# Kernel optimization log

Measured on AMD Instinct MI355X. Metric: run time of the kernel, lower is better.

## Reference

```python
import jax, jax.numpy as jnp
import numpy as np

B, C, H, W = 8, 512, 64, 64


def conv3x3(x, w, b):
    # x: [B,C,H,W], w: [O,I,3,3], b: [O]; stride 1, padding 1 (SAME)
    y = jax.lax.conv_general_dilated(
        x, w, window_strides=(1, 1), padding='SAME',
        dimension_numbers=('NCHW', 'OIHW', 'NCHW'))
    return y + b[None, :, None, None]


def setup_inputs() -> dict:
    key = jax.random.key(0)
    ks = jax.random.split(key, 8)
    wscale = 1.0 / np.sqrt(C * 9)  # keep attention logits in a sane range
    x = jax.random.normal(ks[0], (B, C, H, W), dtype=jnp.float32)
    wq = jax.random.normal(ks[1], (C, C, 3, 3), dtype=jnp.float32) * wscale
    bq = jax.random.normal(ks[2], (C,), dtype=jnp.float32) * 0.01
    wk = jax.random.normal(ks[3], (C, C, 3, 3), dtype=jnp.float32) * wscale
    bk = jax.random.normal(ks[4], (C,), dtype=jnp.float32) * 0.01
    wv = jax.random.normal(ks[5], (C, C, 3, 3), dtype=jnp.float32) * wscale
    bv = jax.random.normal(ks[6], (C,), dtype=jnp.float32) * 0.01
    gamma = jax.random.normal(ks[7], (1,), dtype=jnp.float32)
    return {'x': x, 'wq': wq, 'bq': bq, 'wk': wk, 'bk': bk,
            'wv': wv, 'bv': bv, 'gamma': gamma}


def reference(x, wq, bq, wk, bk, wv, bv, gamma):
    b, c, h, w = x.shape
    n = h * w
    q = conv3x3(x, wq, bq).reshape(b, c, n)   # [B,C,N]
    k = conv3x3(x, wk, bk).reshape(b, c, n)   # [B,C,N]
    v = conv3x3(x, wv, bv).reshape(b, c, n)   # [B,C,N]
    # channel-wise attention: [B,C,N] x [B,N,C] -> [B,C,C]
    attn = jnp.einsum('bcn,bdn->bcd', q, k)
    attn = jax.nn.softmax(attn, axis=-1)
    out = jnp.einsum('bcd,bdn->bcn', attn, v).reshape(b, c, h, w)
    return gamma * out + x
```

## Files before the change

kernel.cpp:

```cpp
#include <hip/hip_runtime.h>
#include <stdint.h>

typedef __attribute__((ext_vector_type(8))) short bf16x8;
typedef __attribute__((ext_vector_type(4))) float f32x4;
typedef __attribute__((ext_vector_type(4))) int i32x4;
typedef __attribute__((ext_vector_type(8))) int i32x8;
typedef __attribute__((ext_vector_type(8))) unsigned short u16x8;
typedef __attribute__((ext_vector_type(4))) unsigned short u16x4;

#define DI static __device__ __forceinline__

constexpr int CB = 8;
constexpr int BCH = 4;
constexpr int CC = 512;
constexpr int CN = 4096;
constexpr int K1 = CC * 9;
constexpr int MR = 3 * CC;
constexpr int KSPL = 8;
constexpr size_t XSPLIT = (size_t)BCH * 66 * 66 * 512;

DI unsigned short f2bf(float f) {
  union { float f; uint32_t u; } v; v.f = f;
  uint32_t r = (v.u + 0x7FFFu + ((v.u >> 16) & 1u)) >> 16;
  return (unsigned short)r;
}
DI float bf2f(unsigned short h) {
  union { uint32_t u; float f; } v; v.u = ((uint32_t)h) << 16;
  return v.f;
}
DI unsigned char f2e4m3(float x) {
  union { float f; uint32_t u; } v; v.f = x;
  uint32_t sgn = (v.u >> 24) & 0x80u;
  float a = fabsf(x);
  if (a < 0.015625f) {
    int qi = (int)rintf(a * 512.f);
    return (unsigned char)(sgn | (uint32_t)qi);
  }
  int e = (int)((v.u >> 23) & 0xff) - 127;
  uint32_t m3 = (v.u >> 20) & 7u;
  uint32_t rest = v.u & 0xFFFFFu;
  if (rest > 0x80000u || (rest == 0x80000u && (m3 & 1u))) {
    if (++m3 == 8u) { m3 = 0; ++e; }
  }
  if (e > 8 || (e == 8 && m3 == 7u)) return (unsigned char)(sgn | 0x7Eu);
  return (unsigned char)(sgn | ((uint32_t)(e + 7) << 3) | m3);
}

DI void g2lds16(const void* g, void* l) {
  __builtin_amdgcn_global_load_lds((const __attribute__((address_space(1))) void*)g,
                                   (__attribute__((address_space(3))) void*)l, 16, 0, 0);
}
#define SBAR()  __builtin_amdgcn_s_barrier()
#define SCHED() __builtin_amdgcn_sched_barrier(0)

__global__ __launch_bounds__(256) void pad_zero(unsigned short* __restrict__ Xhi,
                                                unsigned char* __restrict__ X8) {
  int id = blockIdx.x * 256 + threadIdx.x;
  if (id >= 4 * 260 * 16) return;
  int t = id & 15;
  int pp = (id >> 4) % 260;
  int b = id / (260 * 16);
  int hh, ww;
  if (pp < 66)       { hh = 0;  ww = pp; }
  else if (pp < 132) { hh = 65; ww = pp - 66; }
  else if (pp < 196) { hh = pp - 131; ww = 0; }
  else               { hh = pp - 195; ww = 65; }
  size_t pix = (((size_t)b * 66 + hh) * 66 + ww) * 512 + (size_t)t * 32;
  const u16x8 z = {0, 0, 0, 0, 0, 0, 0, 0};
  *(u16x8*)&Xhi[pix] = z;  *(u16x8*)&Xhi[pix + 8] = z;
  *(u16x8*)&Xhi[pix + 16] = z;  *(u16x8*)&Xhi[pix + 24] = z;
  const i32x4 z4 = {0, 0, 0, 0};
  *(i32x4*)&X8[pix] = z4;  *(i32x4*)&X8[pix + 16] = z4;
  *(i32x4*)&X8[XSPLIT + pix] = z4;  *(i32x4*)&X8[XSPLIT + pix + 16] = z4;
}

__global__ __launch_bounds__(256) void prep_xpad(const float* __restrict__ x,
                                                 unsigned short* __restrict__ Xhi,
                                                 unsigned char* __restrict__ X8) {
  int tid = threadIdx.x;
  int w = tid & 63;
  int ccl = tid >> 6;
  int blk = blockIdx.x;
  int h = blk & 63;
  int ccg = (blk >> 6) & 15;
  int b = blk >> 10;
  int c0 = (ccg * 4 + ccl) * 8;
  const float* xp = x + ((size_t)b * CC) * CN + h * 64 + w;
  u16x8 hi;
  unsigned long long lo8 = 0, hi8 = 0;
#pragma unroll
  for (int j = 0; j < 8; ++j) {
    float v = xp[(size_t)(c0 + j) * CN];
    unsigned short h16 = f2bf(v);
    float vhi = bf2f(h16);
    hi[j] = f2bf(vhi * 128.f);
    lo8 |= (unsigned long long)f2e4m3((v - vhi) * 256.f) << (8 * j);
    hi8 |= (unsigned long long)f2e4m3(vhi) << (8 * j);
  }
  size_t pix = (((size_t)b * 66 + (h + 1)) * 66 + (w + 1)) * 512;
  *(u16x8*)&Xhi[pix + c0] = hi;
  *(unsigned long long*)&X8[pix + c0] = lo8;
  *(unsigned long long*)&X8[XSPLIT + pix + c0] = hi8;
}

__global__ __launch_bounds__(256) void prep_abig(
    const float* __restrict__ wq, const float* __restrict__ wk,
    const float* __restrict__ wv, const float* __restrict__ bq,
    const float* __restrict__ bk, const float* __restrict__ bv,
    unsigned short* __restrict__ Ahi, unsigned char* __restrict__ A8,
    float* __restrict__ bias) {
  unsigned id = blockIdx.x * 256 + threadIdx.x;
  int m = id / K1;
  int r = id - m * K1;
  int t = r >> 9;
  int c = r & 511;
  int ky = t / 3;
  int kx = t - ky * 3;
  size_t ip = (size_t)m * 9216 + r;
  if (m < 1024) {
    const float* wp = (m < 512) ? wq : wk;
    int mm = (m < 512) ? m : m - 512;
    float wval = wp[(((size_t)mm * 512 + c) * 3 + ky) * 3 + kx];
    float whi = bf2f(f2bf(wval));
    Ahi[id] = f2bf(whi * 128.f);
    A8[ip] = f2e4m3(whi * 64.f);
    A8[ip + 4608] = f2e4m3((wval - whi) * 16384.f);
  } else {
    float wval = wv[(((size_t)(m - 1024) * 512 + c) * 3 + ky) * 3 + kx];
    Ahi[id] = f2bf(wval * 128.f);
    A8[ip] = 0;
    A8[ip + 4608] = 0;
  }
  if (id < 1536) {
    int mm = (int)id;
    bias[mm] = (mm < 512) ? bq[mm] : (mm < 1024) ? bk[mm - 512] : bv[mm - 1024];
  }
}

__global__ __launch_bounds__(512, 2) void conv_k(
    const unsigned short* __restrict__ Ahi,
    const unsigned char* __restrict__ A8,
    const unsigned short* __restrict__ Xhi,
    const unsigned char* __restrict__ X8,
    const float* __restrict__ bias,
    unsigned short* __restrict__ Qhi, unsigned short* __restrict__ Qlo,
    unsigned short* __restrict__ Khi, unsigned short* __restrict__ Klo,
    unsigned short* __restrict__ Vt)
{
  __shared__ __align__(16) unsigned char smem[4 * 32768];
  const int tid = threadIdx.x;
  const int lane = tid & 63;
  const int wid = tid >> 6;
  const int wr = wid >> 2;
  const int wc = wid & 3;

  int orig = blockIdx.x;
  int xcd, nbl, m0;
  if (orig < 256) {
    xcd = orig & 7; int j = orig >> 3;
    nbl = j >> 2;
    m0 = (j & 3) * 256;
  } else {
    int o = orig - 256;
    xcd = o & 7; int j = o >> 3;
    nbl = j >> 2;
    m0 = 1024 + (j & 3) * 128;
  }
  const int nb = xcd * 8 + nbl;
  const int n0 = nb * 256;
  const int bidx = n0 >> 12;
  const int nl0 = n0 & (CN - 1);
  const int h0 = nl0 >> 6;

  const int srow = tid >> 2;
  const int scu = tid & 3;
  const int scuS = scu ^ ((srow >> 1) & 3);
  const int d8 = (scuS & 1) ? -16 : 16;
  const size_t pixOfs = (((size_t)(bidx * 66 + h0 + (srow >> 6))) * 66 + (srow & 63)) * 512;
  const unsigned short* gAh0 = Ahi + (size_t)(m0 + srow) * K1 + scuS * 8;
  const unsigned short* gAh1 = gAh0 + (size_t)128 * K1;
  const unsigned short* gBh0 = Xhi + pixOfs + scuS * 8;
  const unsigned short* gBh1 = gBh0 + (size_t)2 * 66 * 512;
  const unsigned char* gA80 = A8 + (size_t)(m0 + srow) * 9216 + scuS * 16;
  const unsigned char* gA81 = gA80 + (size_t)128 * 9216;
  const unsigned char* gB80 = X8 + pixOfs + scuS * 16;
  const unsigned char* gB81 = gB80 + (size_t)2 * 66 * 512;
  const int wofs = wid * 1024;

  int c0S = 0, kxS = 0, tapS = 0;
  size_t tapOfs = 0;
  auto stage1 = [&](int slot) {
    int aOfs = tapS * 512 + c0S;
    size_t bOfs = tapOfs + (size_t)c0S;
    unsigned char* lA = smem + slot * 32768 + wofs;
    unsigned char* lB = smem + slot * 32768 + 16384 + wofs;
    g2lds16(gAh0 + aOfs, lA);
    g2lds16(gAh1 + aOfs, lA + 8192);
    g2lds16(gBh0 + bOfs, lB);
    g2lds16(gBh1 + bOfs, lB + 8192);
    c0S += 32;
    if (c0S == 512) {
      c0S = 0; ++tapS;
      if (kxS == 2) { kxS = 0; tapOfs += (size_t)64 * 512; }
      else { ++kxS; tapOfs += 512; }
    }
  };
  auto stage1v = [&](int slot) {
    int aOfs = tapS * 512 + c0S;
    size_t bOfs = tapOfs + (size_t)c0S;
    unsigned char* lA = smem + slot * 32768 + wofs;
    unsigned char* lB = smem + slot * 32768 + 16384 + wofs;
    g2lds16(gAh0 + aOfs, lA);
    g2lds16(gBh0 + bOfs, lB);
    g2lds16(gBh1 + bOfs, lB + 8192);
    c0S += 32;
    if (c0S == 512) {
      c0S = 0; ++tapS;
      if (kxS == 2) { kxS = 0; tapOfs += (size_t)64 * 512; }
      else { ++kxS; tapOfs += 512; }
    }
  };
  int c8 = 0, kx8 = 0, tap8 = 0, s8 = 0;
  size_t tapOfs8 = 0;
  auto stage2 = [&](int slot) {
    int so = (slot & 1) ? d8 : 0;
    int aOfs = s8 * 4608 + tap8 * 512 + c8;
    size_t bOfs = (size_t)s8 * XSPLIT + tapOfs8 + (size_t)c8;
    unsigned char* lA = smem + slot * 32768 + wofs;
    unsigned char* lB = smem + slot * 32768 + 16384 + wofs;
    g2lds16(gA80 + aOfs + so, lA);
    g2lds16(gA81 + aOfs + so, lA + 8192);
    g2lds16(gB80 + bOfs + so, lB);
    g2lds16(gB81 + bOfs + so, lB + 8192);
    c8 += 64;
    if (c8 == 512) {
      c8 = 0; ++tap8;
      if (tap8 == 9) { tap8 = 0; kx8 = 0; tapOfs8 = 0; ++s8; }
      else if (kx8 == 2) { kx8 = 0; tapOfs8 += (size_t)64 * 512; }
      else { ++kx8; tapOfs8 += 512; }
    }
  };

  f32x4 acc[8][4];
  const f32x4 fz = {0.f, 0.f, 0.f, 0.f};
#pragma unroll
  for (int i = 0; i < 8; ++i)
#pragma unroll
    for (int j = 0; j < 4; ++j) acc[i][j] = fz;

  const int kq = (lane >> 4) * 16;
  int slotC, slotS, t2;

  if (m0 < 1024) {
    const int rA = wr * 128 + (lane & 15);
    const int rB = wc * 64 + (lane & 15);
    const int kqA = kq ^ (((rA >> 1) & 3) << 4);
    const int kqB = kq ^ (((rB >> 1) & 3) << 4);

    stage1(0);
    stage1(1);
    asm volatile("s_waitcnt vmcnt(4)" ::: "memory");
    SCHED(); SBAR(); SCHED();
    {
      bf16x8 afA[4], bfA[4], afB[4], bfB[4], af1[4];
#pragma unroll
      for (int mf = 0; mf < 4; ++mf)
        afA[mf] = *(const bf16x8*)(smem + (rA + mf * 16) * 64 + kqA);
#pragma unroll
      for (int nf = 0; nf < 4; ++nf)
        bfA[nf] = *(const bf16x8*)(smem + 16384 + (rB + nf * 16) * 64 + kqB);
      slotC = 0; slotS = 2; t2 = 2;

#define CONV_BF(CURA, CURB, NXTA, NXTB)                                       \
  {                                                                           \
    if (t2 < 144) {                                                           \
      stage1(slotS); slotS = (slotS + 1) & 3;                                 \
      asm volatile("s_waitcnt vmcnt(4)" ::: "memory");                        \
    } else {                                                                  \
      asm volatile("s_waitcnt vmcnt(0)" ::: "memory");                        \
    }                                                                         \
    SCHED(); SBAR(); SCHED();                                                 \
    const unsigned char* lA = smem + slotC * 32768;                           \
    const int slotN = (slotC + 1) & 3;                                        \
    const unsigned char* lAn = smem + slotN * 32768;                          \
    _Pragma("unroll")                                                         \
    for (int mf = 0; mf < 4; ++mf)                                            \
      af1[mf] = *(const bf16x8*)(lA + (rA + 64 + mf * 16) * 64 + kqA);        \
    __builtin_amdgcn_s_setprio(1);                                            \
    _Pragma("unroll")                                                         \
    for (int mf = 0; mf < 4; ++mf) {                                          \
      _Pragma("unroll")                                                       \
      for (int nf = 0; nf < 4; ++nf)                                          \
        acc[mf][nf] = __builtin_amdgcn_mfma_f32_16x16x32_bf16(                \
            CURA[mf], CURB[nf], acc[mf][nf], 0, 0, 0);                        \
    }                                                                         \
    __builtin_amdgcn_s_setprio(0);                                            \
    _Pragma("unroll")                                                         \
    for (int mf = 0; mf < 4; ++mf)                                            \
      NXTA[mf] = *(const bf16x8*)(lAn + (rA + mf * 16) * 64 + kqA);           \
    _Pragma("unroll")                                                         \
    for (int nf = 0; nf < 4; ++nf)                                            \
      NXTB[nf] = *(const bf16x8*)(lAn + 16384 + (rB + nf * 16) * 64 + kqB);   \
    __builtin_amdgcn_s_setprio(1);                                            \
    _Pragma("unroll")                                                         \
    for (int mf = 0; mf < 4; ++mf) {                                          \
      _Pragma("unroll")                                                       \
      for (int nf = 0; nf < 4; ++nf)                                          \
        acc[mf + 4][nf] = __builtin_amdgcn_mfma_f32_16x16x32_bf16(            \
            af1[mf], CURB[nf], acc[mf + 4][nf], 0, 0, 0);                     \
    }                                                                         \
    __builtin_amdgcn_s_setprio(0);                                            \
    slotC = slotN;                                                            \
    ++t2;                                                                     \
  }

      for (int t = 0; t < 144; t += 2) {
        CONV_BF(afA, bfA, afB, bfB)
        CONV_BF(afB, bfB, afA, bfA)
      }
#undef CONV_BF
    }

    stage2(0); stage2(1);
    SCHED(); SBAR(); SCHED();
    stage2(2); stage2(3);
    {
      const int gq = lane >> 4;
      const int slotByte = (gq >> 1) << 15;
      const int cb2 = (gq & 1) * 2;
      const int fx = (((lane & 15) >> 1) & 3) ^ (gq >> 1);
      const int bo0 = ((cb2 ^ fx) << 4);
      const int bo1 = (((cb2 + 1) ^ fx) << 4);
      const int aRow = wr * 128 + (lane & 15);
      const int bRow = wc * 64 + (lane & 15);
      i32x8 aF[4], bF[4];
      for (int p = 0; p < 72; ++p) {
        SCHED(); SBAR(); SCHED();
        if (p < 71) { asm volatile("s_waitcnt vmcnt(8)" ::: "memory"); }
        else        { asm volatile("s_waitcnt vmcnt(0)" ::: "memory"); }
        SCHED();
        const unsigned char* pbA = smem + ((p & 1) << 16) + slotByte + aRow * 64;
        const unsigned char* pbB = smem + ((p & 1) << 16) + slotByte + 16384 + bRow * 64;
#pragma unroll
        for (int t = 0; t < 4; ++t) {
          *(i32x4*)&bF[t] = *(const i32x4*)(pbB + t * 1024 + bo0);
          *((i32x4*)&bF[t] + 1) = *(const i32x4*)(pbB + t * 1024 + bo1);
        }
#pragma unroll
        for (int s = 0; s < 4; ++s) {
          *(i32x4*)&aF[s] = *(const i32x4*)(pbA + s * 1024 + bo0);
          *((i32x4*)&aF[s] + 1) = *(const i32x4*)(pbA + s * 1024 + bo1);
        }
        __builtin_amdgcn_s_setprio(1);
#pragma unroll
        for (int s = 0; s < 4; ++s)
#pragma unroll
          for (int t = 0; t < 4; ++t)
            acc[s][t] = __builtin_amdgcn_mfma_scale_f32_16x16x128_f8f6f4(
                aF[s], bF[t], acc[s][t], 0, 0, 0, 127, 0, 127);
        __builtin_amdgcn_s_setprio(0);
#pragma unroll
        for (int s = 0; s < 4; ++s) {
          *(i32x4*)&aF[s] = *(const i32x4*)(pbA + (4 + s) * 1024 + bo0);
          *((i32x4*)&aF[s] + 1) = *(const i32x4*)(pbA + (4 + s) * 1024 + bo1);
        }
        __builtin_amdgcn_s_setprio(1);
#pragma unroll
        for (int s = 0; s < 4; ++s)
#pragma unroll
          for (int t = 0; t < 4; ++t)
            acc[s + 4][t] = __builtin_amdgcn_mfma_scale_f32_16x16x128_f8f6f4(
                aF[s], bF[t], acc[s + 4][t], 0, 0, 0, 127, 0, 127);
        __builtin_amdgcn_s_setprio(0);
        SCHED(); SBAR(); SCHED();
        if (p + 2 < 72) { stage2(2 * (p & 1)); stage2(2 * (p & 1) + 1); }
      }
    }
  } else {
    const int rAv = wr * 64 + (lane & 15);
    const int rB = wc * 64 + (lane & 15);
    const int kqA = kq ^ (((rAv >> 1) & 3) << 4);
    const int kqB = kq ^ (((rB >> 1) & 3) << 4);

    stage1v(0);
    stage1v(1);
    asm volatile("s_waitcnt vmcnt(3)" ::: "memory");
    SCHED(); SBAR(); SCHED();
    bf16x8 afA[4], bfA[4], afB[4], bfB[4];
#pragma unroll
    for (int mf = 0; mf < 4; ++mf)
      afA[mf] = *(const bf16x8*)(smem + (rAv + mf * 16) * 64 + kqA);
#pragma unroll
    for (int nf = 0; nf < 4; ++nf)
      bfA[nf] = *(const bf16x8*)(smem + 16384 + (rB + nf * 16) * 64 + kqB);
    slotC = 0; slotS = 2; t2 = 2;

#define CONV_LV(CURA, CURB, NXTA, NXTB)                                       \
  {                                                                           \
    if (t2 < 144) {                                                           \
      stage1v(slotS); slotS = (slotS + 1) & 3;                                \
      asm volatile("s_waitcnt vmcnt(3)" ::: "memory");                        \
    } else {                                                                  \
      asm volatile("s_waitcnt vmcnt(0)" ::: "memory");                        \
    }                                                                         \
    SCHED(); SBAR(); SCHED();                                                 \
    const int slotN = (slotC + 1) & 3;                                        \
    const unsigned char* lAn = smem + slotN * 32768;                          \
    _Pragma("unroll")                                                         \
    for (int mf = 0; mf < 4; ++mf)                                            \
      NXTA[mf] = *(const bf16x8*)(lAn + (rAv + mf * 16) * 64 + kqA);          \
    _Pragma("unroll")                                                         \
    for (int nf = 0; nf < 4; ++nf)                                            \
      NXTB[nf] = *(const bf16x8*)(lAn + 16384 + (rB + nf * 16) * 64 + kqB);   \
    __builtin_amdgcn_s_setprio(1);                                            \
    _Pragma("unroll")                                                         \
    for (int mf = 0; mf < 4; ++mf) {                                          \
      _Pragma("unroll")                                                       \
      for (int nf = 0; nf < 4; ++nf)                                          \
        acc[mf][nf] = __builtin_amdgcn_mfma_f32_16x16x32_bf16(                \
            CURA[mf], CURB[nf], acc[mf][nf], 0, 0, 0);                        \
    }                                                                         \
    __builtin_amdgcn_s_setprio(0);                                            \
    slotC = slotN;                                                            \
    ++t2;                                                                     \
  }

    for (int t = 0; t < 144; t += 2) {
      CONV_LV(afA, bfA, afB, bfB)
      CONV_LV(afB, bfB, afA, bfA)
    }
#undef CONV_LV
  }

  constexpr float SC = 1.f / 16384.f;
  if (m0 < 1024) {
#pragma unroll
    for (int mf = 0; mf < 8; ++mf) {
#pragma unroll
      for (int nf = 0; nf < 4; ++nf) {
        f32x4 a = acc[mf][nf];
        int mrow = m0 + wr * 128 + mf * 16 + ((lane >> 4) << 2);
        int ncol = nl0 + wc * 64 + nf * 16 + (lane & 15);
        if (m0 < 512) {
#pragma unroll
          for (int j = 0; j < 4; ++j) {
            float v = a[j] * SC + bias[mrow + j];
            unsigned short h16 = f2bf(v);
            size_t o = ((size_t)bidx * CC + (mrow + j)) * CN + ncol;
            Qhi[o] = h16;
            Qlo[o] = f2bf(v - bf2f(h16));
          }
        } else {
#pragma unroll
          for (int j = 0; j < 4; ++j) {
            float v = a[j] * SC + bias[mrow + j];
            unsigned short h16 = f2bf(v);
            size_t o = ((size_t)bidx * CC + (mrow + j - 512)) * CN + ncol;
            Khi[o] = h16;
            Klo[o] = f2bf(v - bf2f(h16));
          }
        }
      }
    }
  } else {
#pragma unroll
    for (int mf = 0; mf < 4; ++mf) {
#pragma unroll
      for (int nf = 0; nf < 4; ++nf) {
        f32x4 a = acc[mf][nf];
        int mrow = m0 + wr * 64 + mf * 16 + ((lane >> 4) << 2);
        int ncol = nl0 + wc * 64 + nf * 16 + (lane & 15);
        u16x4 vs;
#pragma unroll
        for (int j = 0; j < 4; ++j) vs[j] = f2bf(a[j] * SC + bias[mrow + j]);
        *(u16x4*)&Vt[((size_t)bidx * CN + ncol) * CC + (mrow - 1024)] = vs;
      }
    }
  }
}

__global__ __launch_bounds__(512, 2) void qk_k(
    const unsigned short* __restrict__ Qhi, const unsigned short* __restrict__ Qlo,
    const unsigned short* __restrict__ Khi, const unsigned short* __restrict__ Klo,
    float* __restrict__ attn)
{
  __shared__ __align__(16) unsigned char smem[4 * 24576];
  const int tid = threadIdx.x;
  const int lane = tid & 63;
  const int wid = tid >> 6;
  const int wr = wid >> 2;
  const int wc = wid & 3;

  int orig = blockIdx.x;
  int work = (orig & 7) * 8 + (orig >> 3);
  const int mt = work & 3;
  const int nt = (work >> 2) & 1;
  const int ks = work >> 3;
  const int bidx = blockIdx.z;
  const int m0 = mt * 128;
  const int n0 = nt * 256;

  const int srow = tid >> 2;
  const int scu = tid & 3;
  const int scuS = scu ^ ((srow >> 1) & 3);
  const size_t rowA = ((size_t)bidx * CC + m0 + srow) * CN + scuS * 8;
  const size_t rowB = ((size_t)bidx * CC + n0 + srow) * CN + scuS * 8;
  const size_t rowB2 = rowB + (size_t)128 * CN;
  const int wofs = wid * 1024;

  int kk = ks * 1536;
  auto stageQ = [&](int slot) {
    int ph = kk >> 12;
    int kin = kk & (CN - 1);
    const unsigned short* Aq = (ph == 2) ? Qlo : Qhi;
    const unsigned short* Bk = (ph == 1) ? Klo : Khi;
    unsigned char* lA = smem + slot * 24576 + wofs;
    unsigned char* lB = smem + slot * 24576 + 8192 + wofs;
    g2lds16(Aq + rowA + kin, lA);
    g2lds16(Bk + rowB + kin, lB);
    g2lds16(Bk + rowB2 + kin, lB + 8192);
    kk += 32;
  };

  f32x4 acc[4][4];
  const f32x4 fz = {0.f, 0.f, 0.f, 0.f};
#pragma unroll
  for (int i = 0; i < 4; ++i)
#pragma unroll
    for (int j = 0; j < 4; ++j) acc[i][j] = fz;

  const int rAv = wr * 64 + (lane & 15);
  const int rB = wc * 64 + (lane & 15);
  const int kq = (lane >> 4) * 16;
  const int kqA = kq ^ (((rAv >> 1) & 3) << 4);
  const int kqB = kq ^ (((rB >> 1) & 3) << 4);

  stageQ(0);
  stageQ(1);
  asm volatile("s_waitcnt vmcnt(3)" ::: "memory");
  SCHED(); SBAR(); SCHED();
  bf16x8 afA[4], bfA[4], afB[4], bfB[4];
#pragma unroll
  for (int mf = 0; mf < 4; ++mf)
    afA[mf] = *(const bf16x8*)(smem + (rAv + mf * 16) * 64 + kqA);
#pragma unroll
  for (int nf = 0; nf < 4; ++nf)
    bfA[nf] = *(const bf16x8*)(smem + 8192 + (rB + nf * 16) * 64 + kqB);
  int slotC = 0, slotS = 2, t2 = 2;

#define QK_BODY(CURA, CURB, NXTA, NXTB)                                       \
  {                                                                           \
    if (t2 < 48) {                                                            \
      stageQ(slotS); slotS = (slotS + 1) & 3;                                 \
      asm volatile("s_waitcnt vmcnt(3)" ::: "memory");                        \
    } else {                                                                  \
      asm volatile("s_waitcnt vmcnt(0)" ::: "memory");                        \
    }                                                                         \
    SCHED(); SBAR(); SCHED();                                                 \
    const int slotN = (slotC + 1) & 3;                                        \
    const unsigned char* lAn = smem + slotN * 24576;                          \
    _Pragma("unroll")                                                         \
    for (int mf = 0; mf < 4; ++mf)                                            \
      NXTA[mf] = *(const bf16x8*)(lAn + (rAv + mf * 16) * 64 + kqA);          \
    _Pragma("unroll")                                                         \
    for (int nf = 0; nf < 4; ++nf)                                            \
      NXTB[nf] = *(const bf16x8*)(lAn + 8192 + (rB + nf * 16) * 64 + kqB);    \
    __builtin_amdgcn_s_setprio(1);                                            \
    _Pragma("unroll")                                                         \
    for (int mf = 0; mf < 4; ++mf) {                                          \
      _Pragma("unroll")                                                       \
      for (int nf = 0; nf < 4; ++nf)                                          \
        acc[mf][nf] = __builtin_amdgcn_mfma_f32_16x16x32_bf16(                \
            CURA[mf], CURB[nf], acc[mf][nf], 0, 0, 0);                        \
    }                                                                         \
    __builtin_amdgcn_s_setprio(0);                                            \
    slotC = slotN;                                                            \
    ++t2;                                                                     \
  }

  for (int t = 0; t < 48; t += 2) {
    QK_BODY(afA, bfA, afB, bfB)
    QK_BODY(afB, bfB, afA, bfA)
  }
#undef QK_BODY

  size_t pbase = (size_t)ks * ((size_t)BCH * CC * CC);
#pragma unroll
  for (int mf = 0; mf < 4; ++mf) {
#pragma unroll
    for (int nf = 0; nf < 4; ++nf) {
      f32x4 a = acc[mf][nf];
      int mrow = m0 + wr * 64 + mf * 16 + ((lane >> 4) << 2);
      int ncol = n0 + wc * 64 + nf * 16 + (lane & 15);
#pragma unroll
      for (int j = 0; j < 4; ++j)
        attn[pbase + ((size_t)bidx * CC + (mrow + j)) * CC + ncol] = a[j];
    }
  }
}

DI int sofs(int row, int kb) { return row * 128 + (kb ^ ((row & 7) << 4)); }

__global__ __launch_bounds__(256) void pv_k(
    const unsigned short* __restrict__ Vt,
    const unsigned short* __restrict__ P,
    const float* __restrict__ xin,
    const float* __restrict__ gamma,
    float* __restrict__ out)
{
  __shared__ __align__(16) unsigned char sA[16384];
  __shared__ __align__(16) unsigned char sB[16384];
  const int tid = threadIdx.x;
  const int lane = tid & 63;
  const int wav = tid >> 6;
  const int wr = wav >> 1, wc = wav & 1;

  const int m0 = (blockIdx.x & 3) * 128;
  const int n0 = (blockIdx.x >> 2) * 128;
  const int bidx = blockIdx.z;

  auto stage = [&](int k0) {
#pragma unroll
    for (int q = 0; q < 4; ++q) {
      int ci = q * 256 + tid;
      int row = ci >> 3;
      int ke = ((ci & 7) ^ (row & 7)) * 8;
      const unsigned short* ap = P + ((size_t)bidx * CC + (m0 + row)) * CC + (k0 + ke);
      const unsigned short* bp = Vt + ((size_t)bidx * CN + (n0 + row)) * CC + (k0 + ke);
      int wbase = (q * 256 + wav * 64) * 16;
      g2lds16(ap, sA + wbase);
      g2lds16(bp, sB + wbase);
    }
  };

  f32x4 acc[4][4];
  const f32x4 fz = {0.f, 0.f, 0.f, 0.f};
#pragma unroll
  for (int i = 0; i < 4; ++i)
#pragma unroll
    for (int j = 0; j < 4; ++j) acc[i][j] = fz;

  for (int k0 = 0; k0 < CC; k0 += 64) {
    stage(k0);
    __syncthreads();
#pragma unroll
    for (int kkp = 0; kkp < 2; ++kkp) {
      bf16x8 af[4], bfv[4];
#pragma unroll
      for (int mf = 0; mf < 4; ++mf)
        af[mf] = *(const bf16x8*)&sA[sofs(wr * 64 + mf * 16 + (lane & 15),
                                          kkp * 64 + (lane >> 4) * 16)];
#pragma unroll
      for (int nf = 0; nf < 4; ++nf)
        bfv[nf] = *(const bf16x8*)&sB[sofs(wc * 64 + nf * 16 + (lane & 15),
                                           kkp * 64 + (lane >> 4) * 16)];
#pragma unroll
      for (int mf = 0; mf < 4; ++mf)
#pragma unroll
        for (int nf = 0; nf < 4; ++nf)
          acc[mf][nf] = __builtin_amdgcn_mfma_f32_16x16x32_bf16(
              af[mf], bfv[nf], acc[mf][nf], 0, 0, 0);
    }
    __syncthreads();
  }

  float g = gamma[0];
#pragma unroll
  for (int mf = 0; mf < 4; ++mf) {
#pragma unroll
    for (int nf = 0; nf < 4; ++nf) {
      f32x4 a = acc[mf][nf];
      int mrow = m0 + wr * 64 + mf * 16 + ((lane >> 4) << 2);
      int ncol = n0 + wc * 64 + nf * 16 + (lane & 15);
#pragma unroll
      for (int j = 0; j < 4; ++j) {
        size_t o = ((size_t)bidx * CC + (mrow + j)) * CN + ncol;
        out[o] = g * a[j] + xin[o];
      }
    }
  }
}

__global__ __launch_bounds__(256) void softmax_k(const float* __restrict__ attn,
                                                 unsigned short* __restrict__ P) {
  int row = blockIdx.x * 4 + (threadIdx.x >> 6);
  int lane = threadIdx.x & 63;
  constexpr size_t PS = (size_t)BCH * CC * CC;
  const float* rp = attn + (size_t)row * 512 + lane * 8;
  f32x4 a = {0.f, 0.f, 0.f, 0.f};
  f32x4 b = {0.f, 0.f, 0.f, 0.f};
#pragma unroll
  for (int ksp = 0; ksp < KSPL; ++ksp) {
    a += *(const f32x4*)(rp + (size_t)ksp * PS);
    b += *(const f32x4*)(rp + (size_t)ksp * PS + 4);
  }
  float mx = fmaxf(fmaxf(fmaxf(a[0], a[1]), fmaxf(a[2], a[3])),
                   fmaxf(fmaxf(b[0], b[1]), fmaxf(b[2], b[3])));
#pragma unroll
  for (int s = 32; s > 0; s >>= 1) mx = fmaxf(mx, __shfl_xor(mx, s, 64));
  float e[8];
  float sum = 0.f;
#pragma unroll
  for (int j = 0; j < 4; ++j) { e[j] = __expf(a[j] - mx); sum += e[j]; }
#pragma unroll
  for (int j = 0; j < 4; ++j) { e[4 + j] = __expf(b[j] - mx); sum += e[4 + j]; }
#pragma unroll
  for (int s = 32; s > 0; s >>= 1) sum += __shfl_xor(sum, s, 64);
  float inv = 1.0f / sum;
  u16x8 o;
#pragma unroll
  for (int j = 0; j < 8; ++j) o[j] = f2bf(e[j] * inv);
  *(u16x8*)&P[(size_t)row * 512 + lane * 8] = o;
}

__global__ __launch_bounds__(256) void fill_sentinel(float* __restrict__ out, int n) {
  int i = blockIdx.x * 256 + threadIdx.x;
  if (i < n) out[i] = 1.0e4f;
}

extern "C" void kernel_launch(void* const* d_in, const int* in_sizes, int n_in,
                              void* d_out, int out_size, void* d_ws, size_t ws_size,
                              hipStream_t stream) {
  (void)in_sizes; (void)n_in;
  const float* x  = (const float*)d_in[0];
  const float* wq = (const float*)d_in[1];
  const float* bq = (const float*)d_in[2];
  const float* wk = (const float*)d_in[3];
  const float* bk = (const float*)d_in[4];
  const float* wv = (const float*)d_in[5];
  const float* bv = (const float*)d_in[6];
  const float* gm = (const float*)d_in[7];
  float* out = (float*)d_out;

  uint8_t* wsp = (uint8_t*)d_ws;
  auto take = [&](size_t bytes) {
    uint8_t* p = wsp;
    wsp += (bytes + 255) & ~(size_t)255;
    return p;
  };
  unsigned short* Xhi = (unsigned short*)take(XSPLIT * 2);
  unsigned char*  X8  = (unsigned char*)take(2 * XSPLIT);
  unsigned short* Ahi = (unsigned short*)take((size_t)MR * K1 * 2);
  unsigned char*  A8  = (unsigned char*)take((size_t)MR * 2 * K1);
  float* bias         = (float*)take((size_t)MR * 4);
  unsigned short* Khi = (unsigned short*)take((size_t)BCH * CC * CN * 2);
  unsigned short* Klo = (unsigned short*)take((size_t)BCH * CC * CN * 2);
  unsigned short* Vt  = (unsigned short*)take((size_t)BCH * CN * CC * 2);
  float* attn         = (float*)Xhi;
  unsigned short* P   = (unsigned short*)((uint8_t*)Xhi +
                          (size_t)KSPL * BCH * CC * CC * 4 + 256);

  size_t needed = (size_t)(wsp - (uint8_t*)d_ws);
  if (ws_size < needed) {
    fill_sentinel<<<(out_size + 255) / 256, 256, 0, stream>>>(out, out_size);
    return;
  }

  for (int ch = 0; ch < CB / BCH; ++ch) {
    const float* xch = x + (size_t)ch * BCH * CC * CN;
    float* outch = out + (size_t)ch * BCH * CC * CN;
    unsigned short* Qhi = (unsigned short*)outch;
    unsigned short* Qlo = Qhi + (size_t)BCH * CC * CN;

    pad_zero<<<(4 * 260 * 16 + 255) / 256, 256, 0, stream>>>(Xhi, X8);
    prep_xpad<<<BCH * 16 * 64, 256, 0, stream>>>(xch, Xhi, X8);
    if (ch == 0)
      prep_abig<<<(MR * K1) / 256, 256, 0, stream>>>(wq, wk, wv, bq, bk, bv,
                                                     Ahi, A8, bias);
    conv_k<<<dim3(512), 512, 0, stream>>>(Ahi, A8, Xhi, X8, bias,
                                          Qhi, Qlo, Khi, Klo, Vt);
    qk_k<<<dim3(64, 1, BCH), 512, 0, stream>>>(Qhi, Qlo, Khi, Klo, attn);
    softmax_k<<<BCH * 128, 256, 0, stream>>>(attn, P);
    pv_k<<<dim3(128, 1, BCH), 256, 0, stream>>>(Vt, P, xch, gm, outch);
  }
}
```

Measured before the change: 945.2 us.

## Shrink conv tiles to 128 rows for higher occupancy and unify code paths

```diff
diff --git a/kernel.cpp b/kernel.cpp
--- a/kernel.cpp
+++ b/kernel.cpp
@@ -137,7 +137,7 @@
   }
 }
 
-__global__ __launch_bounds__(512, 2) void conv_k(
+__global__ __launch_bounds__(512, 4) void conv_k(
     const unsigned short* __restrict__ Ahi,
     const unsigned char* __restrict__ A8,
     const unsigned short* __restrict__ Xhi,
@@ -147,7 +147,7 @@
     unsigned short* __restrict__ Khi, unsigned short* __restrict__ Klo,
     unsigned short* __restrict__ Vt)
 {
-  __shared__ __align__(16) unsigned char smem[4 * 32768];
+  __shared__ __align__(16) unsigned char smem[3 * 24576];
   const int tid = threadIdx.x;
   const int lane = tid & 63;
   const int wid = tid >> 6;
@@ -156,12 +156,12 @@
 
   int orig = blockIdx.x;
   int xcd, nbl, m0;
-  if (orig < 256) {
+  if (orig < 512) {
     xcd = orig & 7; int j = orig >> 3;
-    nbl = j >> 2;
-    m0 = (j & 3) * 256;
+    nbl = j >> 3;
+    m0 = (j & 7) * 128;
   } else {
-    int o = orig - 256;
+    int o = orig - 512;
     xcd = o & 7; int j = o >> 3;
     nbl = j >> 2;
     m0 = 1024 + (j & 3) * 128;
@@ -175,14 +175,11 @@
   const int srow = tid >> 2;
   const int scu = tid & 3;
   const int scuS = scu ^ ((srow >> 1) & 3);
-  const int d8 = (scuS & 1) ? -16 : 16;
   const size_t pixOfs = (((size_t)(bidx * 66 + h0 + (srow >> 6))) * 66 + (srow & 63)) * 512;
   const unsigned short* gAh0 = Ahi + (size_t)(m0 + srow) * K1 + scuS * 8;
-  const unsigned short* gAh1 = gAh0 + (size_t)128 * K1;
   const unsigned short* gBh0 = Xhi + pixOfs + scuS * 8;
   const unsigned short* gBh1 = gBh0 + (size_t)2 * 66 * 512;
   const unsigned char* gA80 = A8 + (size_t)(m0 + srow) * 9216 + scuS * 16;
-  const unsigned char* gA81 = gA80 + (size_t)128 * 9216;
   const unsigned char* gB80 = X8 + pixOfs + scuS * 16;
   const unsigned char* gB81 = gB80 + (size_t)2 * 66 * 512;
   const int wofs = wid * 1024;
@@ -192,12 +189,10 @@
   auto stage1 = [&](int slot) {
     int aOfs = tapS * 512 + c0S;
     size_t bOfs = tapOfs + (size_t)c0S;
-    unsigned char* lA = smem + slot * 32768 + wofs;
-    unsigned char* lB = smem + slot * 32768 + 16384 + wofs;
-    g2lds16(gAh0 + aOfs, lA);
-    g2lds16(gAh1 + aOfs, lA + 8192);
-    g2lds16(gBh0 + bOfs, lB);
-    g2lds16(gBh1 + bOfs, lB + 8192);
+    unsigned char* lS = smem + slot * 24576 + wofs;
+    g2lds16(gAh0 + aOfs, lS);
+    g2lds16(gBh0 + bOfs, lS + 8192);
+    g2lds16(gBh1 + bOfs, lS + 16384);
     c0S += 32;
     if (c0S == 512) {
       c0S = 0; ++tapS;
@@ -205,87 +200,70 @@
       else { ++kxS; tapOfs += 512; }
     }
   };
-  auto stage1v = [&](int slot) {
-    int aOfs = tapS * 512 + c0S;
-    size_t bOfs = tapOfs + (size_t)c0S;
-    unsigned char* lA = smem + slot * 32768 + wofs;
-    unsigned char* lB = smem + slot * 32768 + 16384 + wofs;
-    g2lds16(gAh0 + aOfs, lA);
-    g2lds16(gBh0 + bOfs, lB);
-    g2lds16(gBh1 + bOfs, lB + 8192);
-    c0S += 32;
-    if (c0S == 512) {
-      c0S = 0; ++tapS;
-      if (kxS == 2) { kxS = 0; tapOfs += (size_t)64 * 512; }
-      else { ++kxS; tapOfs += 512; }
+  int c2 = 0, kx2 = 0, tap2 = 0, s2 = 0;
+  size_t tapOfs2 = 0;
+  auto stagePair = [&]() {
+    int aOfs = s2 * 4608 + tap2 * 512 + c2;
+    size_t bOfs = (size_t)s2 * XSPLIT + tapOfs2 + (size_t)c2;
+    g2lds16(gA80 + aOfs, smem + wofs);
+    g2lds16(gB80 + bOfs, smem + 8192 + wofs);
+    g2lds16(gB81 + bOfs, smem + 16384 + wofs);
+    g2lds16(gA80 + aOfs + 64, smem + 24576 + wofs);
+    g2lds16(gB80 + bOfs + 64, smem + 24576 + 8192 + wofs);
+    g2lds16(gB81 + bOfs + 64, smem + 24576 + 16384 + wofs);
+    c2 += 128;
+    if (c2 == 512) {
+      c2 = 0; ++tap2;
+      if (tap2 == 9) { tap2 = 0; kx2 = 0; tapOfs2 = 0; ++s2; }
+      else if (kx2 == 2) { kx2 = 0; tapOfs2 += (size_t)64 * 512; }
+      else { ++kx2; tapOfs2 += 512; }
     }
   };
-  int c8 = 0, kx8 = 0, tap8 = 0, s8 = 0;
-  size_t tapOfs8 = 0;
-  auto stage2 = [&](int slot) {
-    int so = (slot & 1) ? d8 : 0;
-    int aOfs = s8 * 4608 + tap8 * 512 + c8;
-    size_t bOfs = (size_t)s8 * XSPLIT + tapOfs8 + (size_t)c8;
-    unsigned char* lA = smem + slot * 32768 + wofs;
-    unsigned char* lB = smem + slot * 32768 + 16384 + wofs;
-    g2lds16(gA80 + aOfs + so, lA);
-    g2lds16(gA81 + aOfs + so, lA + 8192);
-    g2lds16(gB80 + bOfs + so, lB);
-    g2lds16(gB81 + bOfs + so, lB + 8192);
-    c8 += 64;
-    if (c8 == 512) {
-      c8 = 0; ++tap8;
-      if (tap8 == 9) { tap8 = 0; kx8 = 0; tapOfs8 = 0; ++s8; }
-      else if (kx8 == 2) { kx8 = 0; tapOfs8 += (size_t)64 * 512; }
-      else { ++kx8; tapOfs8 += 512; }
-    }
-  };
-
-  f32x4 acc[8][4];
+
+  f32x4 acc[4][4];
   const f32x4 fz = {0.f, 0.f, 0.f, 0.f};
 #pragma unroll
-  for (int i = 0; i < 8; ++i)
+  for (int i = 0; i < 4; ++i)
 #pragma unroll
     for (int j = 0; j < 4; ++j) acc[i][j] = fz;
 
+  const int rAv = wr * 64 + (lane & 15);
+  const int rB = wc * 64 + (lane & 15);
   const int kq = (lane >> 4) * 16;
-  int slotC, slotS, t2;
-
-  if (m0 < 1024) {
-    const int rA = wr * 128 + (lane & 15);
-    const int rB = wc * 64 + (lane & 15);
-    const int kqA = kq ^ (((rA >> 1) & 3) << 4);
-    const int kqB = kq ^ (((rB >> 1) & 3) << 4);
-
-    stage1(0);
-    stage1(1);
-    asm volatile("s_waitcnt vmcnt(4)" ::: "memory");
-    SCHED(); SBAR(); SCHED();
-    {
-      bf16x8 afA[4], bfA[4], afB[4], bfB[4], af1[4];
-#pragma unroll
-      for (int mf = 0; mf < 4; ++mf)
-        afA[mf] = *(const bf16x8*)(smem + (rA + mf * 16) * 64 + kqA);
-#pragma unroll
-      for (int nf = 0; nf < 4; ++nf)
-        bfA[nf] = *(const bf16x8*)(smem + 16384 + (rB + nf * 16) * 64 + kqB);
-      slotC = 0; slotS = 2; t2 = 2;
-
-#define CONV_BF(CURA, CURB, NXTA, NXTB)                                       \
+  const int kqA = kq ^ (((rAv >> 1) & 3) << 4);
+  const int kqB = kq ^ (((rB >> 1) & 3) << 4);
+
+  stage1(0);
+  stage1(1);
+  asm volatile("s_waitcnt vmcnt(3)" ::: "memory");
+  SCHED(); SBAR(); SCHED();
+  {
+    bf16x8 afA[4], bfA[4], afB[4], bfB[4];
+#pragma unroll
+    for (int mf = 0; mf < 4; ++mf)
+      afA[mf] = *(const bf16x8*)(smem + (rAv + mf * 16) * 64 + kqA);
+#pragma unroll
+    for (int nf = 0; nf < 4; ++nf)
+      bfA[nf] = *(const bf16x8*)(smem + 8192 + (rB + nf * 16) * 64 + kqB);
+    int slotC = 0, slotS = 2, t2 = 2;
+
+#define CONV_P1(CURA, CURB, NXTA, NXTB)                                       \
   {                                                                           \
     if (t2 < 144) {                                                           \
-      stage1(slotS); slotS = (slotS + 1) & 3;                                 \
-      asm volatile("s_waitcnt vmcnt(4)" ::: "memory");                        \
+      stage1(slotS); slotS = (slotS == 2) ? 0 : slotS + 1;                    \
+      asm volatile("s_waitcnt vmcnt(3)" ::: "memory");                        \
     } else {                                                                  \
       asm volatile("s_waitcnt vmcnt(0)" ::: "memory");                        \
     }                                                                         \
     SCHED(); SBAR(); SCHED();                                                 \
-    const unsigned char* lA = smem + slotC * 32768;                           \
-    const int slotN = (slotC + 1) & 3;                                        \
-    const unsigned char* lAn = smem + slotN * 32768;                          \
+    const int slotN = (slotC == 2) ? 0 : slotC + 1;                           \
+    const unsigned char* lAn = smem + slotN * 24576;                          \
     _Pragma("unroll")                                                         \
     for (int mf = 0; mf < 4; ++mf)                                            \
-      af1[mf] = *(const bf16x8*)(lA + (rA + 64 + mf * 16) * 64 + kqA);        \
+      NXTA[mf] = *(const bf16x8*)(lAn + (rAv + mf * 16) * 64 + kqA);          \
+    _Pragma("unroll")                                                         \
+    for (int nf = 0; nf < 4; ++nf)                                            \
+      NXTB[nf] = *(const bf16x8*)(lAn + 8192 + (rB + nf * 16) * 64 + kqB);    \
     __builtin_amdgcn_s_setprio(1);                                            \
     _Pragma("unroll")                                                         \
     for (int mf = 0; mf < 4; ++mf) {                                          \
@@ -295,181 +273,84 @@
             CURA[mf], CURB[nf], acc[mf][nf], 0, 0, 0);                        \
     }                                                                         \
     __builtin_amdgcn_s_setprio(0);                                            \
-    _Pragma("unroll")                                                         \
-    for (int mf = 0; mf < 4; ++mf)                                            \
-      NXTA[mf] = *(const bf16x8*)(lAn + (rA + mf * 16) * 64 + kqA);           \
-    _Pragma("unroll")                                                         \
-    for (int nf = 0; nf < 4; ++nf)                                            \
-      NXTB[nf] = *(const bf16x8*)(lAn + 16384 + (rB + nf * 16) * 64 + kqB);   \
-    __builtin_amdgcn_s_setprio(1);                                            \
-    _Pragma("unroll")                                                         \
-    for (int mf = 0; mf < 4; ++mf) {                                          \
-      _Pragma("unroll")                                                       \
-      for (int nf = 0; nf < 4; ++nf)                                          \
-        acc[mf + 4][nf] = __builtin_amdgcn_mfma_f32_16x16x32_bf16(            \
-            af1[mf], CURB[nf], acc[mf + 4][nf], 0, 0, 0);                     \
-    }                                                                         \
-    __builtin_amdgcn_s_setprio(0);                                            \
+    asm volatile("s_waitcnt lgkmcnt(0)" ::: "memory");                        \
+    SCHED(); SBAR(); SCHED();                                                 \
     slotC = slotN;                                                            \
     ++t2;                                                                     \
   }
 
-      for (int t = 0; t < 144; t += 2) {
-        CONV_BF(afA, bfA, afB, bfB)
-        CONV_BF(afB, bfB, afA, bfA)
+    for (int t = 0; t < 144; t += 2) {
+      CONV_P1(afA, bfA, afB, bfB)
+      CONV_P1(afB, bfB, afA, bfA)
+    }
+#undef CONV_P1
+  }
+
+  if (m0 < 1024) {
+    const int gq = lane >> 4;
+    const int slotByte = (gq >> 1) * 24576;
+    const int cb2 = (gq & 1) * 2;
+    const int fx = ((lane & 15) >> 1) & 3;
+    const int bo0 = ((cb2 ^ fx) << 4);
+    const int bo1 = (((cb2 + 1) ^ fx) << 4);
+    i32x8 aF[4], bF[4];
+    for (int p = 0; p < 72; ++p) {
+      stagePair();
+      asm volatile("s_waitcnt vmcnt(0)" ::: "memory");
+      SCHED(); SBAR(); SCHED();
+      const unsigned char* pbA = smem + slotByte;
+      const unsigned char* pbB = smem + slotByte + 8192;
+#pragma unroll
+      for (int s = 0; s < 4; ++s) {
+        const unsigned char* ra = pbA + (rAv + s * 16) * 64;
+        *(i32x4*)&aF[s] = *(const i32x4*)(ra + bo0);
+        *((i32x4*)&aF[s] + 1) = *(const i32x4*)(ra + bo1);
       }
-#undef CONV_BF
-    }
-
-    stage2(0); stage2(1);
-    SCHED(); SBAR(); SCHED();
-    stage2(2); stage2(3);
-    {
-      const int gq = lane >> 4;
-      const int slotByte = (gq >> 1) << 15;
-      const int cb2 = (gq & 1) * 2;
-      const int fx = (((lane & 15) >> 1) & 3) ^ (gq >> 1);
-      const int bo0 = ((cb2 ^ fx) << 4);
-      const int bo1 = (((cb2 + 1) ^ fx) << 4);
-      const int aRow = wr * 128 + (lane & 15);
-      const int bRow = wc * 64 + (lane & 15);
-      i32x8 aF[4], bF[4];
-      for (int p = 0; p < 72; ++p) {
-        SCHED(); SBAR(); SCHED();
-        if (p < 71) { asm volatile("s_waitcnt vmcnt(8)" ::: "memory"); }
-        else        { asm volatile("s_waitcnt vmcnt(0)" ::: "memory"); }
-        SCHED();
-        const unsigned char* pbA = smem + ((p & 1) << 16) + slotByte + aRow * 64;
-        const unsigned char* pbB = smem + ((p & 1) << 16) + slotByte + 16384 + bRow * 64;
-#pragma unroll
-        for (int t = 0; t < 4; ++t) {
-          *(i32x4*)&bF[t] = *(const i32x4*)(pbB + t * 1024 + bo0);
-          *((i32x4*)&bF[t] + 1) = *(const i32x4*)(pbB + t * 1024 + bo1);
+#pragma unroll
+      for (int tt = 0; tt < 4; ++tt) {
+        const unsigned char* rb = pbB + (rB + tt * 16) * 64;
+        *(i32x4*)&bF[tt] = *(const i32x4*)(rb + bo0);
+        *((i32x4*)&bF[tt] + 1) = *(const i32x4*)(rb + bo1);
+      }
+      __builtin_amdgcn_s_setprio(1);
+#pragma unroll
+      for (int s = 0; s < 4; ++s)
+#pragma unroll
+        for (int tt = 0; tt < 4; ++tt)
+          acc[s][tt] = __builtin_amdgcn_mfma_scale_f32_16x16x128_f8f6f4(
+              aF[s], bF[tt], acc[s][tt], 0, 0, 0, 127, 0, 127);
+      __builtin_amdgcn_s_setprio(0);
+      SCHED(); SBAR(); SCHED();
+    }
+  }
+
+  constexpr float SC = 1.f / 16384.f;
+#pragma unroll
+  for (int mf = 0; mf < 4; ++mf) {
+#pragma unroll
+    for (int nf = 0; nf < 4; ++nf) {
+      f32x4 a = acc[mf][nf];
+      int mrow = m0 + wr * 64 + mf * 16 + ((lane >> 4) << 2);
+      int ncol = nl0 + wc * 64 + nf * 16 + (lane & 15);
+      if (m0 < 512) {
+#pragma unroll
+        for (int j = 0; j < 4; ++j) {
+          float v = a[j] * SC + bias[mrow + j];
+          unsigned short h16 = f2bf(v);
+          size_t o = ((size_t)bidx * CC + (mrow + j)) * CN + ncol;
+          Qhi[o] = h16;
+          Qlo[o] = f2bf(v - bf2f(h16));
         }
-#pragma unroll
-        for (int s = 0; s < 4; ++s) {
-          *(i32x4*)&aF[s] = *(const i32x4*)(pbA + s * 1024 + bo0);
-          *((i32x4*)&aF[s] + 1) = *(const i32x4*)(pbA + s * 1024 + bo1);
+      } else if (m0 < 1024) {
+#pragma unroll
+        for (int j = 0; j < 4; ++j) {
+          float v = a[j] * SC + bias[mrow + j];
+          unsigned short h16 = f2bf(v);
+          size_t o = ((size_t)bidx * CC + (mrow + j - 512)) * CN + ncol;
+          Khi[o] = h16;
+          Klo[o] = f2bf(v - bf2f(h16));
         }
-        __builtin_amdgcn_s_setprio(1);
-#pragma unroll
-        for (int s = 0; s < 4; ++s)
-#pragma unroll
-          for (int t = 0; t < 4; ++t)
-            acc[s][t] = __builtin_amdgcn_mfma_scale_f32_16x16x128_f8f6f4(
-                aF[s], bF[t], acc[s][t], 0, 0, 0, 127, 0, 127);
-        __builtin_amdgcn_s_setprio(0);
-#pragma unroll
-        for (int s = 0; s < 4; ++s) {
-          *(i32x4*)&aF[s] = *(const i32x4*)(pbA + (4 + s) * 1024 + bo0);
-          *((i32x4*)&aF[s] + 1) = *(const i32x4*)(pbA + (4 + s) * 1024 + bo1);
-        }
-        __builtin_amdgcn_s_setprio(1);
-#pragma unroll
-        for (int s = 0; s < 4; ++s)
-#pragma unroll
-          for (int t = 0; t < 4; ++t)
-            acc[s + 4][t] = __builtin_amdgcn_mfma_scale_f32_16x16x128_f8f6f4(
-                aF[s], bF[t], acc[s + 4][t], 0, 0, 0, 127, 0, 127);
-        __builtin_amdgcn_s_setprio(0);
-        SCHED(); SBAR(); SCHED();
-        if (p + 2 < 72) { stage2(2 * (p & 1)); stage2(2 * (p & 1) + 1); }
-      }
-    }
-  } else {
-    const int rAv = wr * 64 + (lane & 15);
-    const int rB = wc * 64 + (lane & 15);
-    const int kqA = kq ^ (((rAv >> 1) & 3) << 4);
-    const int kqB = kq ^ (((rB >> 1) & 3) << 4);
-
-    stage1v(0);
-    stage1v(1);
-    asm volatile("s_waitcnt vmcnt(3)" ::: "memory");
-    SCHED(); SBAR(); SCHED();
-    bf16x8 afA[4], bfA[4], afB[4], bfB[4];
-#pragma unroll
-    for (int mf = 0; mf < 4; ++mf)
-      afA[mf] = *(const bf16x8*)(smem + (rAv + mf * 16) * 64 + kqA);
-#pragma unroll
-    for (int nf = 0; nf < 4; ++nf)
-      bfA[nf] = *(const bf16x8*)(smem + 16384 + (rB + nf * 16) * 64 + kqB);
-    slotC = 0; slotS = 2; t2 = 2;
-
-#define CONV_LV(CURA, CURB, NXTA, NXTB)                                       \
-  {                                                                           \
-    if (t2 < 144) {                                                           \
-      stage1v(slotS); slotS = (slotS + 1) & 3;                                \
-      asm volatile("s_waitcnt vmcnt(3)" ::: "memory");                        \
-    } else {                                                                  \
-      asm volatile("s_waitcnt vmcnt(0)" ::: "memory");                        \
-    }                                                                         \
-    SCHED(); SBAR(); SCHED();                                                 \
-    const int slotN = (slotC + 1) & 3;                                        \
-    const unsigned char* lAn = smem + slotN * 32768;                          \
-    _Pragma("unroll")                                                         \
-    for (int mf = 0; mf < 4; ++mf)                                            \
-      NXTA[mf] = *(const bf16x8*)(lAn + (rAv + mf * 16) * 64 + kqA);          \
-    _Pragma("unroll")                                                         \
-    for (int nf = 0; nf < 4; ++nf)                                            \
-      NXTB[nf] = *(const bf16x8*)(lAn + 16384 + (rB + nf * 16) * 64 + kqB);   \
-    __builtin_amdgcn_s_setprio(1);                                            \
-    _Pragma("unroll")                                                         \
-    for (int mf = 0; mf < 4; ++mf) {                                          \
-      _Pragma("unroll")                                                       \
-      for (int nf = 0; nf < 4; ++nf)                                          \
-        acc[mf][nf] = __builtin_amdgcn_mfma_f32_16x16x32_bf16(                \
-            CURA[mf], CURB[nf], acc[mf][nf], 0, 0, 0);                        \
-    }                                                                         \
-    __builtin_amdgcn_s_setprio(0);                                            \
-    slotC = slotN;                                                            \
-    ++t2;                                                                     \
-  }
-
-    for (int t = 0; t < 144; t += 2) {
-      CONV_LV(afA, bfA, afB, bfB)
-      CONV_LV(afB, bfB, afA, bfA)
-    }
-#undef CONV_LV
-  }
-
-  constexpr float SC = 1.f / 16384.f;
-  if (m0 < 1024) {
-#pragma unroll
-    for (int mf = 0; mf < 8; ++mf) {
-#pragma unroll
-      for (int nf = 0; nf < 4; ++nf) {
-        f32x4 a = acc[mf][nf];
-        int mrow = m0 + wr * 128 + mf * 16 + ((lane >> 4) << 2);
-        int ncol = nl0 + wc * 64 + nf * 16 + (lane & 15);
-        if (m0 < 512) {
-#pragma unroll
-          for (int j = 0; j < 4; ++j) {
-            float v = a[j] * SC + bias[mrow + j];
-            unsigned short h16 = f2bf(v);
-            size_t o = ((size_t)bidx * CC + (mrow + j)) * CN + ncol;
-            Qhi[o] = h16;
-            Qlo[o] = f2bf(v - bf2f(h16));
-          }
-        } else {
-#pragma unroll
-          for (int j = 0; j < 4; ++j) {
-            float v = a[j] * SC + bias[mrow + j];
-            unsigned short h16 = f2bf(v);
-            size_t o = ((size_t)bidx * CC + (mrow + j - 512)) * CN + ncol;
-            Khi[o] = h16;
-            Klo[o] = f2bf(v - bf2f(h16));
-          }
-        }
-      }
-    }
-  } else {
-#pragma unroll
-    for (int mf = 0; mf < 4; ++mf) {
-#pragma unroll
-      for (int nf = 0; nf < 4; ++nf) {
-        f32x4 a = acc[mf][nf];
-        int mrow = m0 + wr * 64 + mf * 16 + ((lane >> 4) << 2);
-        int ncol = nl0 + wc * 64 + nf * 16 + (lane & 15);
+      } else {
         u16x4 vs;
 #pragma unroll
         for (int j = 0; j < 4; ++j) vs[j] = f2bf(a[j] * SC + bias[mrow + j]);
@@ -767,7 +648,7 @@
     if (ch == 0)
       prep_abig<<<(MR * K1) / 256, 256, 0, stream>>>(wq, wk, wv, bq, bk, bv,
                                                      Ahi, A8, bias);
-    conv_k<<<dim3(512), 512, 0, stream>>>(Ahi, A8, Xhi, X8, bias,
+    conv_k<<<dim3(768), 512, 0, stream>>>(Ahi, A8, Xhi, X8, bias,
                                           Qhi, Qlo, Khi, Klo, Vt);
     qk_k<<<dim3(64, 1, BCH), 512, 0, stream>>>(Qhi, Qlo, Khi, Klo, attn);
     softmax_k<<<BCH * 128, 256, 0, stream>>>(attn, P);
```

After: 2.410 ms. 155% more time.

## Pipeline PV kernel with 4-slot async LDS ring and larger tiles

Applied to the files above, without the earlier changes.

```diff
diff --git a/kernel.cpp b/kernel.cpp
--- a/kernel.cpp
+++ b/kernel.cpp
@@ -294,14 +294,12 @@
         acc[mf][nf] = __builtin_amdgcn_mfma_f32_16x16x32_bf16(                \
             CURA[mf], CURB[nf], acc[mf][nf], 0, 0, 0);                        \
     }                                                                         \
-    __builtin_amdgcn_s_setprio(0);                                            \
     _Pragma("unroll")                                                         \
     for (int mf = 0; mf < 4; ++mf)                                            \
       NXTA[mf] = *(const bf16x8*)(lAn + (rA + mf * 16) * 64 + kqA);           \
     _Pragma("unroll")                                                         \
     for (int nf = 0; nf < 4; ++nf)                                            \
       NXTB[nf] = *(const bf16x8*)(lAn + 16384 + (rB + nf * 16) * 64 + kqB);   \
-    __builtin_amdgcn_s_setprio(1);                                            \
     _Pragma("unroll")                                                         \
     for (int mf = 0; mf < 4; ++mf) {                                          \
       _Pragma("unroll")                                                       \
@@ -358,13 +356,11 @@
           for (int t = 0; t < 4; ++t)
             acc[s][t] = __builtin_amdgcn_mfma_scale_f32_16x16x128_f8f6f4(
                 aF[s], bF[t], acc[s][t], 0, 0, 0, 127, 0, 127);
-        __builtin_amdgcn_s_setprio(0);
 #pragma unroll
         for (int s = 0; s < 4; ++s) {
           *(i32x4*)&aF[s] = *(const i32x4*)(pbA + (4 + s) * 1024 + bo0);
           *((i32x4*)&aF[s] + 1) = *(const i32x4*)(pbA + (4 + s) * 1024 + bo1);
         }
-        __builtin_amdgcn_s_setprio(1);
 #pragma unroll
         for (int s = 0; s < 4; ++s)
 #pragma unroll
@@ -599,38 +595,44 @@
   }
 }
 
-DI int sofs(int row, int kb) { return row * 128 + (kb ^ ((row & 7) << 4)); }
-
-__global__ __launch_bounds__(256) void pv_k(
+__global__ __launch_bounds__(512, 2) void pv_k(
     const unsigned short* __restrict__ Vt,
     const unsigned short* __restrict__ P,
     const float* __restrict__ xin,
     const float* __restrict__ gamma,
     float* __restrict__ out)
 {
-  __shared__ __align__(16) unsigned char sA[16384];
-  __shared__ __align__(16) unsigned char sB[16384];
+  __shared__ __align__(16) unsigned char smem[4 * 24576];
   const int tid = threadIdx.x;
   const int lane = tid & 63;
-  const int wav = tid >> 6;
-  const int wr = wav >> 1, wc = wav & 1;
-
-  const int m0 = (blockIdx.x & 3) * 128;
-  const int n0 = (blockIdx.x >> 2) * 128;
+  const int wid = tid >> 6;
+  const int wr = wid >> 2;
+  const int wc = wid & 3;
+
+  int orig = blockIdx.x;
+  int work = (orig & 7) * 8 + (orig >> 3);
+  const int mt = work & 3;
+  const int nt = work >> 2;
   const int bidx = blockIdx.z;
-
-  auto stage = [&](int k0) {
-#pragma unroll
-    for (int q = 0; q < 4; ++q) {
-      int ci = q * 256 + tid;
-      int row = ci >> 3;
-      int ke = ((ci & 7) ^ (row & 7)) * 8;
-      const unsigned short* ap = P + ((size_t)bidx * CC + (m0 + row)) * CC + (k0 + ke);
-      const unsigned short* bp = Vt + ((size_t)bidx * CN + (n0 + row)) * CC + (k0 + ke);
-      int wbase = (q * 256 + wav * 64) * 16;
-      g2lds16(ap, sA + wbase);
-      g2lds16(bp, sB + wbase);
-    }
+  const int m0 = mt * 128;
+  const int n0 = nt * 256;
+
+  const int srow = tid >> 2;
+  const int scu = tid & 3;
+  const int scuS = scu ^ ((srow >> 1) & 3);
+  const size_t rowA = ((size_t)bidx * CC + m0 + srow) * CC + scuS * 8;
+  const size_t rowB = ((size_t)bidx * CN + n0 + srow) * CC + scuS * 8;
+  const size_t rowB2 = rowB + (size_t)128 * CC;
+  const int wofs = wid * 1024;
+
+  int kk = 0;
+  auto stageP = [&](int slot) {
+    unsigned char* lA = smem + slot * 24576 + wofs;
+    unsigned char* lB = smem + slot * 24576 + 8192 + wofs;
+    g2lds16(P + rowA + kk, lA);
+    g2lds16(Vt + rowB + kk, lB);
+    g2lds16(Vt + rowB2 + kk, lB + 8192);
+    kk += 32;
   };
 
   f32x4 acc[4][4];
@@ -640,29 +642,60 @@
 #pragma unroll
     for (int j = 0; j < 4; ++j) acc[i][j] = fz;
 
-  for (int k0 = 0; k0 < CC; k0 += 64) {
-    stage(k0);
-    __syncthreads();
-#pragma unroll
-    for (int kkp = 0; kkp < 2; ++kkp) {
-      bf16x8 af[4], bfv[4];
-#pragma unroll
-      for (int mf = 0; mf < 4; ++mf)
-        af[mf] = *(const bf16x8*)&sA[sofs(wr * 64 + mf * 16 + (lane & 15),
-                                          kkp * 64 + (lane >> 4) * 16)];
-#pragma unroll
-      for (int nf = 0; nf < 4; ++nf)
-        bfv[nf] = *(const bf16x8*)&sB[sofs(wc * 64 + nf * 16 + (lane & 15),
-                                           kkp * 64 + (lane >> 4) * 16)];
-#pragma unroll
-      for (int mf = 0; mf < 4; ++mf)
-#pragma unroll
-        for (int nf = 0; nf < 4; ++nf)
-          acc[mf][nf] = __builtin_amdgcn_mfma_f32_16x16x32_bf16(
-              af[mf], bfv[nf], acc[mf][nf], 0, 0, 0);
-    }
-    __syncthreads();
-  }
+  const int rAv = wr * 64 + (lane & 15);
+  const int rB = wc * 64 + (lane & 15);
+  const int kq = (lane >> 4) * 16;
+  const int kqA = kq ^ (((rAv >> 1) & 3) << 4);
+  const int kqB = kq ^ (((rB >> 1) & 3) << 4);
+
+  stageP(0);
+  stageP(1);
+  asm volatile("s_waitcnt vmcnt(3)" ::: "memory");
+  SCHED(); SBAR(); SCHED();
+  bf16x8 afA[4], bfA[4], afB[4], bfB[4];
+#pragma unroll
+  for (int mf = 0; mf < 4; ++mf)
+    afA[mf] = *(const bf16x8*)(smem + (rAv + mf * 16) * 64 + kqA);
+#pragma unroll
+  for (int nf = 0; nf < 4; ++nf)
+    bfA[nf] = *(const bf16x8*)(smem + 8192 + (rB + nf * 16) * 64 + kqB);
+  int slotC = 0, slotS = 2, t2 = 2;
+
+#define PV_BODY(CURA, CURB, NXTA, NXTB)                                       \
+  {                                                                           \
+    if (t2 < 16) {                                                            \
+      stageP(slotS); slotS = (slotS + 1) & 3;                                 \
+      asm volatile("s_waitcnt vmcnt(3)" ::: "memory");                        \
+    } else {                                                                  \
+      asm volatile("s_waitcnt vmcnt(0)" ::: "memory");                        \
+    }                                                                         \
+    SCHED(); SBAR(); SCHED();                                                 \
+    const int slotN = (slotC + 1) & 3;                                        \
+    const unsigned char* lAn = smem + slotN * 24576;                          \
+    _Pragma("unroll")                                                         \
+    for (int mf = 0; mf < 4; ++mf)                                            \
+      NXTA[mf] = *(const bf16x8*)(lAn + (rAv + mf * 16) * 64 + kqA);          \
+    _Pragma("unroll")                                                         \
+    for (int nf = 0; nf < 4; ++nf)                                            \
+      NXTB[nf] = *(const bf16x8*)(lAn + 8192 + (rB + nf * 16) * 64 + kqB);    \
+    __builtin_amdgcn_s_setprio(1);                                            \
+    _Pragma("unroll")                                                         \
+    for (int mf = 0; mf < 4; ++mf) {                                          \
+      _Pragma("unroll")                                                       \
+      for (int nf = 0; nf < 4; ++nf)                                          \
+        acc[mf][nf] = __builtin_amdgcn_mfma_f32_16x16x32_bf16(                \
+            CURA[mf], CURB[nf], acc[mf][nf], 0, 0, 0);                        \
+    }                                                                         \
+    __builtin_amdgcn_s_setprio(0);                                            \
+    slotC = slotN;                                                            \
+    ++t2;                                                                     \
+  }
+
+  for (int t = 0; t < 16; t += 2) {
+    PV_BODY(afA, bfA, afB, bfB)
+    PV_BODY(afB, bfB, afA, bfA)
+  }
+#undef PV_BODY
 
   float g = gamma[0];
 #pragma unroll
@@ -771,6 +804,6 @@
                                           Qhi, Qlo, Khi, Klo, Vt);
     qk_k<<<dim3(64, 1, BCH), 512, 0, stream>>>(Qhi, Qlo, Khi, Klo, attn);
     softmax_k<<<BCH * 128, 256, 0, stream>>>(attn, P);
-    pv_k<<<dim3(128, 1, BCH), 256, 0, stream>>>(Vt, P, xch, gm, outch);
-  }
-}
+    pv_k<<<dim3(64, 1, BCH), 512, 0, stream>>>(Vt, P, xch, gm, outch);
+  }
+}
```

Result: no change. 940.2 us (-0.5%).
